# Performance work log

Hardware: AMD Instinct MI355X
Metric: run time of the kernel (lower is better)

Reference implementation:

```python
import jax, jax.numpy as jnp
import numpy as np

B, S, E, H = 4, 1024, 1024, 16
HD = E // H
SCALE = HD ** -0.5


def setup_inputs() -> dict:
    key = jax.random.key(0)
    ks = jax.random.split(key, 10)
    std = E ** -0.5
    return {
        "sequence_embeddings": jax.random.normal(ks[0], (B, S, E), jnp.float32),
        "graph_embeddings": jax.random.normal(ks[1], (B, S, HD), jnp.float32),
        "Wq": jax.random.normal(ks[2], (E, E), jnp.float32) * std,
        "bq": jnp.zeros((E,), jnp.float32),
        "Wk": jax.random.normal(ks[3], (E, E), jnp.float32) * std,
        "bk": jnp.zeros((E,), jnp.float32),
        "Wv": jax.random.normal(ks[4], (E, E), jnp.float32) * std,
        "bv": jnp.zeros((E,), jnp.float32),
        "Wo": jax.random.normal(ks[5], (E, E), jnp.float32) * std,
        "bo": jnp.zeros((E,), jnp.float32),
    }


def reference(sequence_embeddings, graph_embeddings, Wq, bq, Wk, bk, Wv, bv, Wo, bo):
    b, s, e = sequence_embeddings.shape
    # project and split heads: [b, h, s, hd]
    def heads(x, W, bias):
        return (x @ W + bias).reshape(b, s, H, HD).transpose(0, 2, 1, 3)

    q = heads(sequence_embeddings, Wq, bq)
    k = heads(sequence_embeddings, Wk, bk)
    v = heads(sequence_embeddings, Wv, bv)

    # sequence-to-sequence attention: [b, h, s, s]
    attn_scores = jnp.einsum("bhqd,bhkd->bhqk", q, k) * SCALE
    seq_attn = jax.nn.softmax(attn_scores, axis=-1)

    # graph-to-sequence attention: graph [b, s, hd] broadcast over heads -> [b, h, s, s]
    graph_scores = jnp.einsum("bqd,bhkd->bhqk", graph_embeddings, k)
    graph_attn = jax.nn.softmax(graph_scores, axis=-1)

    # fused dual-softmax weights (dropout is identity in eval)
    attn_weights = seq_attn * graph_attn

    attn_out = jnp.einsum("bhqk,bhkd->bhqd", attn_weights, v)
    attn_out = attn_out.transpose(0, 2, 1, 3).reshape(b, s, e)
    output = attn_out @ Wo + bo
    return output, attn_weights
```

## Files before the change

### kernel.cpp

```cpp
#include <hip/hip_runtime.h>
#include <math.h>

#define B_ 4
#define S_ 1024
#define E_ 1024
#define H_ 16
#define HD_ 64

#define LOG2E 1.4426950408889634f
#define C16L2 23.08312065422341f
#define C64L2 92.33248261689365f
#define C80L2 115.41560327111706f

typedef float4 f4;
typedef _Float16 f16x8 __attribute__((ext_vector_type(8)));
typedef ushort u16x8 __attribute__((ext_vector_type(8)));
typedef float f32x4 __attribute__((ext_vector_type(4)));

__device__ __forceinline__ void gl16(const void* g, void* l) {
  __builtin_amdgcn_global_load_lds(
      (__attribute__((address_space(1))) void*)g,
      (__attribute__((address_space(3))) void*)l, 16, 0, 0);
}

__device__ __forceinline__ ushort f2h(float x) {
  return __builtin_bit_cast(ushort, (_Float16)x);
}
__device__ __forceinline__ float h2f(ushort h) {
  return (float)__builtin_bit_cast(_Float16, h);
}
__device__ __forceinline__ float exp2r(float x) {
  return __builtin_amdgcn_exp2f(x);
}
__device__ __forceinline__ f32x4 mfma16(u16x8 a, u16x8 b, f32x4 c) {
  return __builtin_amdgcn_mfma_f32_16x16x32_f16(
      __builtin_bit_cast(f16x8, a), __builtin_bit_cast(f16x8, b), c, 0, 0, 0);
}
__device__ __forceinline__ u16x8 ldfrag(const ushort* s, int row, int chunk) {
  return *reinterpret_cast<const u16x8*>(s + row * 64 + ((chunk ^ (row & 7)) << 3));
}
__device__ __forceinline__ u16x8 ldfrag32(const ushort* s, int row, int chunk) {
  return *reinterpret_cast<const u16x8*>(s + row * 32 + ((chunk ^ (row & 3)) << 3));
}


__global__ __launch_bounds__(256) void prep_x(
    const float* __restrict__ x, ushort* __restrict__ xf)
{
  const size_t i = ((size_t)blockIdx.x * 256 + threadIdx.x) * 8;
  float v[8];
  *reinterpret_cast<f4*>(v)     = *reinterpret_cast<const f4*>(x + i);
  *reinterpret_cast<f4*>(v + 4) = *reinterpret_cast<const f4*>(x + i + 4);
  unsigned fw[4];
#pragma unroll
  for (int p = 0; p < 4; ++p)
    fw[p] = (unsigned)f2h(v[2 * p]) | ((unsigned)f2h(v[2 * p + 1]) << 16);
  *reinterpret_cast<uint4*>(xf + i) = make_uint4(fw[0], fw[1], fw[2], fw[3]);
}

__global__ __launch_bounds__(256) void prep_w(
    const float* __restrict__ Wq, const float* __restrict__ Wk,
    const float* __restrict__ Wv, const float* __restrict__ Wo,
    ushort* __restrict__ ws16)
{
  const int MSZ = 1024 * 1024;
  const int mat = blockIdx.z;
  const int n0 = blockIdx.x * 64, k0 = blockIdx.y * 64;
  const float* W = mat == 0 ? Wq : mat == 1 ? Wk : mat == 2 ? Wv : Wo;
  ushort* Oh = ws16 + (size_t)mat * MSZ;

  __shared__ __align__(16) float tile[64][65];
  const int t = threadIdx.x;
  const int r = t >> 2, cq = t & 3;
#pragma unroll
  for (int j = 0; j < 4; ++j) {
    const f4 v = *reinterpret_cast<const f4*>(&W[(size_t)(k0 + r) * 1024 + n0 + cq * 16 + 4 * j]);
    tile[r][cq * 16 + 4 * j + 0] = v.x;
    tile[r][cq * 16 + 4 * j + 1] = v.y;
    tile[r][cq * 16 + 4 * j + 2] = v.z;
    tile[r][cq * 16 + 4 * j + 3] = v.w;
  }
  __syncthreads();
  unsigned hw[8];
#pragma unroll
  for (int p = 0; p < 8; ++p)
    hw[p] = (unsigned)f2h(tile[cq * 16 + 2 * p][r]) |
            ((unsigned)f2h(tile[cq * 16 + 2 * p + 1][r]) << 16);
  ushort* dh = Oh + (size_t)(n0 + r) * 1024 + k0 + cq * 16;
  *reinterpret_cast<uint4*>(dh)     = make_uint4(hw[0], hw[1], hw[2], hw[3]);
  *reinterpret_cast<uint4*>(dh + 8) = make_uint4(hw[4], hw[5], hw[6], hw[7]);
}

template <int OMODE>
__global__ __launch_bounds__(256) void gemm_mfma(
    const ushort* __restrict__ Ab, const ushort* __restrict__ Bhg,
    const float* __restrict__ bias, float scale,
    ushort* __restrict__ Oh, float* __restrict__ Of)
{
  const int n0 = blockIdx.x * 128;
  const int m0 = blockIdx.y * 64;
  const int t = threadIdx.x;
  const int wv = t >> 6, lane = t & 63;
  const int lr = lane & 15, lg = lane >> 4;
  const int wm = (wv >> 1) * 32, wn = (wv & 1) * 64;
  const int row8 = lane >> 3, ch8 = lane & 7;

  __shared__ __align__(16) ushort Ah_s[64 * 64];
  __shared__ __align__(16) ushort Bh_s[128 * 64];
  __shared__ __align__(16) ushort tr_s[OMODE == 2 ? 128 * 72 : 16];

  f32x4 acc[2][4];
#pragma unroll
  for (int mi = 0; mi < 2; ++mi)
#pragma unroll
    for (int ni = 0; ni < 4; ++ni) { f32x4 z = {0.f, 0.f, 0.f, 0.f}; acc[mi][ni] = z; }

  for (int kt = 0; kt < 16; ++kt) {
    const int k0 = kt * 64;
    __syncthreads();
#pragma unroll
    for (int j = 0; j < 4; ++j) {
      const int row = wv * 32 + j * 8 + row8;
      gl16(Bhg + (size_t)(n0 + row) * 1024 + k0 + ((ch8 ^ (row & 7)) << 3),
           &Bh_s[(wv * 32 + j * 8) * 64]);
    }
#pragma unroll
    for (int j = 0; j < 2; ++j) {
      const int row = wv * 16 + j * 8 + row8;
      gl16(Ab + (size_t)(m0 + row) * 1024 + k0 + ((ch8 ^ (row & 7)) << 3),
           &Ah_s[(wv * 16 + j * 8) * 64]);
    }
    __syncthreads();
#pragma unroll
    for (int ks = 0; ks < 2; ++ks) {
      const u16x8 ah0 = ldfrag(Ah_s, wm + lr, ks * 4 + lg);
      const u16x8 ah1 = ldfrag(Ah_s, wm + 16 + lr, ks * 4 + lg);
#pragma unroll
      for (int ni = 0; ni < 4; ++ni) {
        const u16x8 bh = ldfrag(Bh_s, wn + ni * 16 + lr, ks * 4 + lg);
        acc[0][ni] = mfma16(ah0, bh, acc[0][ni]);
        acc[1][ni] = mfma16(ah1, bh, acc[1][ni]);
      }
    }
  }

  if constexpr (OMODE == 2) {
    __syncthreads();
#pragma unroll
    for (int mi = 0; mi < 2; ++mi)
#pragma unroll
      for (int ni = 0; ni < 4; ++ni)
#pragma unroll
        for (int r = 0; r < 4; ++r) {
          const int n_l = wn + ni * 16 + lr, m_l = wm + mi * 16 + lg * 4 + r;
          tr_s[n_l * 72 + m_l] = f2h(acc[mi][ni][r] + bias[n0 + n_l]);
        }
    __syncthreads();
    const int row = t >> 1, hf = t & 1;
    const int n_g = n0 + row;
    const int h_ = n_g >> 6, hd = n_g & 63;
    const int b_g = m0 >> 10;
    ushort* dst = Oh + ((size_t)(b_g * 16 + h_) * 64 + hd) * 1024 + (m0 & 1023) + hf * 32;
#pragma unroll
    for (int j = 0; j < 4; ++j)
      *reinterpret_cast<uint4*>(dst + 8 * j) =
          *reinterpret_cast<const uint4*>(&tr_s[row * 72 + hf * 32 + 8 * j]);
  } else {
#pragma unroll
    for (int mi = 0; mi < 2; ++mi)
#pragma unroll
      for (int ni = 0; ni < 4; ++ni) {
        const int n = n0 + wn + ni * 16 + lr;
        const float bi = bias[n];
#pragma unroll
        for (int r = 0; r < 4; ++r) {
          const int m = m0 + wm + mi * 16 + lg * 4 + r;
          const float v = (acc[mi][ni][r] + bi) * scale;
          if constexpr (OMODE == 0) {
            Of[(size_t)m * 1024 + n] = v;
          } else {
            const size_t addr =
                ((size_t)((m >> 10) * 16 + (n >> 6)) * 1024 + (m & 1023)) * 64 + (n & 63);
            Oh[addr] = f2h(v);
          }
        }
      }
  }
}

__global__ __launch_bounds__(256) void attn_mfma(
    const ushort* __restrict__ qh_g, const ushort* __restrict__ kf_g,
    const ushort* __restrict__ vt_g, const float* __restrict__ ge,
    float* __restrict__ attn, ushort* __restrict__ aoh)
{
  __shared__ __align__(16) ushort kh2_s[2][2048];
  __shared__ __align__(16) ushort vt2_s[2][2048];
  __shared__ __align__(16) ushort w_s[4][1024];

  const int bid = blockIdx.x;
  const int wg = (bid & 7) * 128 + (bid >> 3);
  const int bh = wg >> 4, qb = wg & 15;
  const int b = bh >> 4, h = bh & 15;

  const int t = threadIdx.x;
  const int wv = t >> 6, lane = t & 63;
  const int lr = lane & 15, lg = lane >> 4;
  const int q0 = qb * 64 + wv * 16;

  u16x8 qh[2], gh[2];
  float gf[2][8];
#pragma unroll
  for (int ks = 0; ks < 2; ++ks) {
    const size_t qoff = ((size_t)bh * S_ + q0 + lr) * HD_ + ks * 32 + lg * 8;
    qh[ks] = *reinterpret_cast<const u16x8*>(qh_g + qoff);
    const float* grow = ge + ((size_t)b * S_ + q0 + lr) * HD_ + ks * 32 + lg * 8;
    f4 g0 = *reinterpret_cast<const f4*>(grow);
    f4 g1 = *reinterpret_cast<const f4*>(grow + 4);
    gf[ks][0] = g0.x * LOG2E; gf[ks][1] = g0.y * LOG2E;
    gf[ks][2] = g0.z * LOG2E; gf[ks][3] = g0.w * LOG2E;
    gf[ks][4] = g1.x * LOG2E; gf[ks][5] = g1.y * LOG2E;
    gf[ks][6] = g1.z * LOG2E; gf[ks][7] = g1.w * LOG2E;
#pragma unroll
    for (int e = 0; e < 8; ++e) gh[ks][e] = f2h(gf[ks][e]);
  }

  const ushort* kfb = kf_g + (size_t)bh * S_ * HD_;
  const ushort* vtb = vt_g + (size_t)bh * HD_ * S_;

  const int krow = wv * 8 + (lane >> 3);
  const int ksw  = ((lane & 7) ^ (krow & 7)) << 3;
  const int vrow = wv * 16 + (lane >> 2);
  const int vsw  = ((lane & 3) ^ (vrow & 3)) << 3;

  auto stage_kf = [&](int kt, int c) {
    gl16(kfb + kt * 2048 + krow * 64 + ksw, &kh2_s[c][wv * 512]);
  };
  auto stage_vt = [&](int kt, int c) {
    gl16(vtb + kt * 32 + (size_t)vrow * 1024 + vsw, &vt2_s[c][wv * 512]);
  };

  float z1L[4] = {0.f, 0.f, 0.f, 0.f}, z2L[4] = {0.f, 0.f, 0.f, 0.f};

  asm volatile("s_waitcnt vmcnt(0)" ::: "memory");
  __builtin_amdgcn_sched_barrier(0);

  stage_kf(0, 0);
  for (int kt = 0; kt < 32; ++kt) {
    if (kt < 31) {
      stage_kf(kt + 1, (kt + 1) & 1);
      asm volatile("s_waitcnt vmcnt(1)" ::: "memory");
    } else {
      asm volatile("s_waitcnt vmcnt(0)" ::: "memory");
    }
    __builtin_amdgcn_sched_barrier(0);
    __builtin_amdgcn_s_barrier();
    __builtin_amdgcn_sched_barrier(0);

    const ushort* kp = kh2_s[kt & 1];
    f32x4 s1[2], s2[2];
#pragma unroll
    for (int ct = 0; ct < 2; ++ct) {
      f32x4 z = {0.f, 0.f, 0.f, 0.f};
      s1[ct] = z; s2[ct] = z;
#pragma unroll
      for (int ks = 0; ks < 2; ++ks) {
        const u16x8 kf = ldfrag(kp, ct * 16 + lr, ks * 4 + lg);
        s1[ct] = mfma16(qh[ks], kf, s1[ct]);
        s2[ct] = mfma16(gh[ks], kf, s2[ct]);
      }
    }
#pragma unroll
    for (int r = 0; r < 4; ++r)
#pragma unroll
      for (int ct = 0; ct < 2; ++ct) {
        z1L[r] += exp2r(s1[ct][r] - C16L2);
        z2L[r] += exp2r(s2[ct][r] - C64L2);
      }
    __builtin_amdgcn_s_barrier();
    __builtin_amdgcn_sched_barrier(0);
  }

  float rzr[4];
#pragma unroll
  for (int r = 0; r < 4; ++r) {
    float z1 = z1L[r], z2 = z2L[r];
#pragma unroll
    for (int msk = 1; msk < 16; msk <<= 1) {
      z1 += __shfl_xor(z1, msk);
      z2 += __shfl_xor(z2, msk);
    }
    rzr[r] = 1.f / (z1 * z2);
  }

  stage_kf(0, 0);
  stage_vt(0, 0);

  u16x8 uh[2];
#pragma unroll
  for (int ks = 0; ks < 2; ++ks)
#pragma unroll
    for (int e = 0; e < 8; ++e)
      uh[ks][e] = f2h(h2f(qh[ks][e]) + gf[ks][e]);

  f32x4 o[4];
#pragma unroll
  for (int dt = 0; dt < 4; ++dt) { f32x4 z = {0.f, 0.f, 0.f, 0.f}; o[dt] = z; }

  float* wrow = attn + ((size_t)bh * S_ + q0) * S_;
  ushort* wsw = w_s[wv];

  for (int kt = 0; kt < 32; ++kt) {
    if (kt < 31) {
      stage_kf(kt + 1, (kt + 1) & 1);
      stage_vt(kt + 1, (kt + 1) & 1);
      if (kt == 0) asm volatile("s_waitcnt vmcnt(2)" ::: "memory");
      else         asm volatile("s_waitcnt vmcnt(4)" ::: "memory");
    } else {
      asm volatile("s_waitcnt vmcnt(2)" ::: "memory");
    }
    __builtin_amdgcn_sched_barrier(0);
    __builtin_amdgcn_s_barrier();
    __builtin_amdgcn_sched_barrier(0);

    const int c = kt & 1;
    const ushort* kfp = kh2_s[c];
    const ushort* vtp = vt2_s[c];

    f32x4 s12[2];
#pragma unroll
    for (int ct = 0; ct < 2; ++ct) {
      f32x4 z = {0.f, 0.f, 0.f, 0.f};
      s12[ct] = z;
#pragma unroll
      for (int ks = 0; ks < 2; ++ks) {
        const u16x8 kf = ldfrag(kfp, ct * 16 + lr, ks * 4 + lg);
        s12[ct] = mfma16(uh[ks], kf, s12[ct]);
      }
    }
#pragma unroll
    for (int ct = 0; ct < 2; ++ct) {
#pragma unroll
      for (int r = 0; r < 4; ++r) {
        const int rowq = lg * 4 + r;
        const int key = ct * 16 + lr;
        const float wv2 = exp2r(s12[ct][r] - C80L2) * rzr[r];
        const int ch = (key >> 3) ^ (rowq & 7);
        wsw[rowq * 64 + ch * 8 + (key & 7)] = f2h(wv2);
      }
    }
    {
      const u16x8 af = ldfrag(wsw, lr, lg);
#pragma unroll
      for (int dt = 0; dt < 4; ++dt) {
        const u16x8 vf = ldfrag32(vtp, dt * 16 + lr, lg);
        o[dt] = mfma16(af, vf, o[dt]);
      }
    }
    {
      const int rowq = lane >> 2, cc = lane & 3;
      const int ch = cc ^ (rowq & 7);
      const uint4 wb = *reinterpret_cast<const uint4*>(&wsw[rowq * 64 + ch * 8]);
      const ushort* wp = reinterpret_cast<const ushort*>(&wb);
      float* dst = wrow + (size_t)rowq * S_ + kt * 32 + cc * 8;
      *reinterpret_cast<f4*>(dst) = make_float4(
          h2f(wp[0]), h2f(wp[1]), h2f(wp[2]), h2f(wp[3]));
      *reinterpret_cast<f4*>(dst + 4) = make_float4(
          h2f(wp[4]), h2f(wp[5]), h2f(wp[6]), h2f(wp[7]));
    }
    __builtin_amdgcn_s_barrier();
    __builtin_amdgcn_sched_barrier(0);
  }

#pragma unroll
  for (int dt = 0; dt < 4; ++dt)
#pragma unroll
    for (int r = 0; r < 4; ++r)
      aoh[((size_t)b * S_ + q0 + lg * 4 + r) * E_ + h * 64 + dt * 16 + lr] =
          f2h(o[dt][r]);
}

extern "C" void kernel_launch(void* const* d_in, const int* in_sizes, int n_in,
                              void* d_out, int out_size, void* d_ws, size_t ws_size,
                              hipStream_t stream) {
  const float* x  = (const float*)d_in[0];
  const float* ge = (const float*)d_in[1];
  const float* Wq = (const float*)d_in[2];
  const float* bq = (const float*)d_in[3];
  const float* Wk = (const float*)d_in[4];
  const float* bk = (const float*)d_in[5];
  const float* Wv = (const float*)d_in[6];
  const float* bv = (const float*)d_in[7];
  const float* Wo = (const float*)d_in[8];
  const float* bo = (const float*)d_in[9];

  float* out  = (float*)d_out;
  float* attn = out + (size_t)B_ * S_ * E_;

  const size_t MSZ = 1024 * 1024;
  ushort* ws16 = (ushort*)d_ws;
  ushort* Wqf = ws16 + 0 * MSZ;
  ushort* Wkf = ws16 + 1 * MSZ;
  ushort* Wvf = ws16 + 2 * MSZ;
  ushort* Wof = ws16 + 3 * MSZ;
  ushort* xf  = ws16 + 4 * MSZ;
  ushort* qh  = ws16 + 8 * MSZ;
  ushort* kf  = ws16 + 12 * MSZ;
  ushort* vt  = ws16 + 16 * MSZ;
  ushort* aoh = ws16 + 20 * MSZ;

  dim3 blk(256);
  hipLaunchKernelGGL(prep_x, dim3(2048), blk, 0, stream, x, xf);
  hipLaunchKernelGGL(prep_w, dim3(16, 16, 4), blk, 0, stream, Wq, Wk, Wv, Wo, ws16);

  dim3 ggrid(E_ / 128, (B_ * S_) / 64);
  hipLaunchKernelGGL((gemm_mfma<3>), ggrid, blk, 0, stream,
                     xf, Wqf, bq, 0.125f * LOG2E, qh, nullptr);
  hipLaunchKernelGGL((gemm_mfma<3>), ggrid, blk, 0, stream,
                     xf, Wkf, bk, 1.0f, kf, nullptr);
  hipLaunchKernelGGL((gemm_mfma<2>), ggrid, blk, 0, stream,
                     xf, Wvf, bv, 1.0f, vt, nullptr);

  hipLaunchKernelGGL(attn_mfma, dim3(1024), blk, 0, stream,
                     qh, kf, vt, ge, attn, aoh);

  hipLaunchKernelGGL((gemm_mfma<0>), ggrid, blk, 0, stream,
                     aoh, Wof, bo, 1.0f, nullptr, out);
}
```

Baseline: 180.1 us.

## Swap MFMA operand order so P stays in registers for PV

Computes the score tiles transposed (K as the A operand, Q as B), so each lane's scores land in the layout the PV MFMA needs as its A operand. The softmax weights are packed directly into the A fragment instead of going through an LDS round-trip. The per-row softmax sums collapse to one scalar per lane, reduced with two shuffles instead of four. The attention-weight output is now staged in an fp32 LDS buffer, so the stored weights keep full precision rather than being fp16-rounded. s_setprio is also raised around the MFMA groups.

```diff
diff --git a/kernel.cpp b/kernel.cpp
--- a/kernel.cpp
+++ b/kernel.cpp
@@ -195,7 +195,7 @@
 {
   __shared__ __align__(16) ushort kh2_s[2][2048];
   __shared__ __align__(16) ushort vt2_s[2][2048];
-  __shared__ __align__(16) ushort w_s[4][1024];
+  __shared__ __align__(16) float w_sf[4][512];
 
   const int bid = blockIdx.x;
   const int wg = (bid & 7) * 128 + (bid >> 3);
@@ -239,7 +239,7 @@
     gl16(vtb + kt * 32 + (size_t)vrow * 1024 + vsw, &vt2_s[c][wv * 512]);
   };
 
-  float z1L[4] = {0.f, 0.f, 0.f, 0.f}, z2L[4] = {0.f, 0.f, 0.f, 0.f};
+  float z1L = 0.f, z2L = 0.f;
 
   asm volatile("s_waitcnt vmcnt(0)" ::: "memory");
   __builtin_amdgcn_sched_barrier(0);
@@ -258,39 +258,35 @@
 
     const ushort* kp = kh2_s[kt & 1];
     f32x4 s1[2], s2[2];
+    __builtin_amdgcn_s_setprio(1);
 #pragma unroll
     for (int ct = 0; ct < 2; ++ct) {
       f32x4 z = {0.f, 0.f, 0.f, 0.f};
       s1[ct] = z; s2[ct] = z;
 #pragma unroll
       for (int ks = 0; ks < 2; ++ks) {
-        const u16x8 kf = ldfrag(kp, ct * 16 + lr, ks * 4 + lg);
-        s1[ct] = mfma16(qh[ks], kf, s1[ct]);
-        s2[ct] = mfma16(gh[ks], kf, s2[ct]);
+        const u16x8 kA = ldfrag(kp, ct * 16 + lr, ks * 4 + lg);
+        s1[ct] = mfma16(kA, qh[ks], s1[ct]);
+        s2[ct] = mfma16(kA, gh[ks], s2[ct]);
       }
     }
-#pragma unroll
-    for (int r = 0; r < 4; ++r)
-#pragma unroll
-      for (int ct = 0; ct < 2; ++ct) {
-        z1L[r] += exp2r(s1[ct][r] - C16L2);
-        z2L[r] += exp2r(s2[ct][r] - C64L2);
+    __builtin_amdgcn_s_setprio(0);
+#pragma unroll
+    for (int ct = 0; ct < 2; ++ct)
+#pragma unroll
+      for (int r = 0; r < 4; ++r) {
+        z1L += exp2r(s1[ct][r] - C16L2);
+        z2L += exp2r(s2[ct][r] - C64L2);
       }
     __builtin_amdgcn_s_barrier();
     __builtin_amdgcn_sched_barrier(0);
   }
 
-  float rzr[4];
-#pragma unroll
-  for (int r = 0; r < 4; ++r) {
-    float z1 = z1L[r], z2 = z2L[r];
-#pragma unroll
-    for (int msk = 1; msk < 16; msk <<= 1) {
-      z1 += __shfl_xor(z1, msk);
-      z2 += __shfl_xor(z2, msk);
-    }
-    rzr[r] = 1.f / (z1 * z2);
-  }
+  float z1 = z1L + __shfl_xor(z1L, 16);
+  z1 += __shfl_xor(z1, 32);
+  float z2 = z2L + __shfl_xor(z2L, 16);
+  z2 += __shfl_xor(z2, 32);
+  const float rz = 1.f / (z1 * z2);
 
   stage_kf(0, 0);
   stage_vt(0, 0);
@@ -307,7 +303,8 @@
   for (int dt = 0; dt < 4; ++dt) { f32x4 z = {0.f, 0.f, 0.f, 0.f}; o[dt] = z; }
 
   float* wrow = attn + ((size_t)bh * S_ + q0) * S_;
-  ushort* wsw = w_s[wv];
+  float* wsw = w_sf[wv];
+  const int prowBase = ((lr >> 2) << 3) | (lr & 3);
 
   for (int kt = 0; kt < 32; ++kt) {
     if (kt < 31) {
@@ -327,45 +324,52 @@
     const ushort* vtp = vt2_s[c];
 
     f32x4 s12[2];
-#pragma unroll
-    for (int ct = 0; ct < 2; ++ct) {
+    {
       f32x4 z = {0.f, 0.f, 0.f, 0.f};
-      s12[ct] = z;
-#pragma unroll
-      for (int ks = 0; ks < 2; ++ks) {
-        const u16x8 kf = ldfrag(kfp, ct * 16 + lr, ks * 4 + lg);
-        s12[ct] = mfma16(uh[ks], kf, s12[ct]);
+      s12[0] = z; s12[1] = z;
+    }
+    __builtin_amdgcn_s_setprio(1);
+#pragma unroll
+    for (int ks = 0; ks < 2; ++ks) {
+      const u16x8 kA0 = ldfrag(kfp, prowBase, ks * 4 + lg);
+      const u16x8 kA1 = ldfrag(kfp, prowBase | 4, ks * 4 + lg);
+      s12[0] = mfma16(kA0, uh[ks], s12[0]);
+      s12[1] = mfma16(kA1, uh[ks], s12[1]);
+    }
+    __builtin_amdgcn_s_setprio(0);
+
+    float wv2[2][4];
+    u16x8 af;
+#pragma unroll
+    for (int ct = 0; ct < 2; ++ct)
+#pragma unroll
+      for (int r = 0; r < 4; ++r) {
+        wv2[ct][r] = exp2r(s12[ct][r] - C80L2) * rz;
+        af[ct * 4 + r] = f2h(wv2[ct][r]);
       }
-    }
-#pragma unroll
-    for (int ct = 0; ct < 2; ++ct) {
-#pragma unroll
-      for (int r = 0; r < 4; ++r) {
-        const int rowq = lg * 4 + r;
-        const int key = ct * 16 + lr;
-        const float wv2 = exp2r(s12[ct][r] - C80L2) * rzr[r];
-        const int ch = (key >> 3) ^ (rowq & 7);
-        wsw[rowq * 64 + ch * 8 + (key & 7)] = f2h(wv2);
-      }
-    }
+
+    __builtin_amdgcn_s_setprio(1);
+#pragma unroll
+    for (int dt = 0; dt < 4; ++dt) {
+      const u16x8 vf = ldfrag32(vtp, dt * 16 + lr, lg);
+      o[dt] = mfma16(af, vf, o[dt]);
+    }
+    __builtin_amdgcn_s_setprio(0);
+
+#pragma unroll
+    for (int ct = 0; ct < 2; ++ct)
+#pragma unroll
+      for (int r = 0; r < 4; ++r)
+        wsw[lr * 32 + lg * 8 + ((ct * 4 + r) ^ (lr & 7))] = wv2[ct][r];
     {
-      const u16x8 af = ldfrag(wsw, lr, lg);
-#pragma unroll
-      for (int dt = 0; dt < 4; ++dt) {
-        const u16x8 vf = ldfrag32(vtp, dt * 16 + lr, lg);
-        o[dt] = mfma16(af, vf, o[dt]);
-      }
-    }
-    {
-      const int rowq = lane >> 2, cc = lane & 3;
-      const int ch = cc ^ (rowq & 7);
-      const uint4 wb = *reinterpret_cast<const uint4*>(&wsw[rowq * 64 + ch * 8]);
-      const ushort* wp = reinterpret_cast<const ushort*>(&wb);
-      float* dst = wrow + (size_t)rowq * S_ + kt * 32 + cc * 8;
-      *reinterpret_cast<f4*>(dst) = make_float4(
-          h2f(wp[0]), h2f(wp[1]), h2f(wp[2]), h2f(wp[3]));
-      *reinterpret_cast<f4*>(dst + 4) = make_float4(
-          h2f(wp[4]), h2f(wp[5]), h2f(wp[6]), h2f(wp[7]));
+      const int rowq = lane >> 2, kc = lane & 3;
+      float vs[8];
+#pragma unroll
+      for (int j = 0; j < 8; ++j)
+        vs[j] = wsw[rowq * 32 + kc * 8 + (j ^ (rowq & 7))];
+      float* dst = wrow + (size_t)rowq * S_ + kt * 32 + kc * 8;
+      *reinterpret_cast<f4*>(dst)     = make_float4(vs[0], vs[1], vs[2], vs[3]);
+      *reinterpret_cast<f4*>(dst + 4) = make_float4(vs[4], vs[5], vs[6], vs[7]);
     }
     __builtin_amdgcn_s_barrier();
     __builtin_amdgcn_sched_barrier(0);
```

After: 182.9 us. Within noise of the previous version (+1.5%).
